# Performance work log

Measured on AMD Instinct MI355X. Metric: run time of the kernel, lower is better.

The kernel has to match this reference:

```python
import jax, jax.numpy as jnp
import numpy as np

E = 1024
FF = 4096
B, S = 4, 2048
EPS = 1e-5

def _layernorm(x, g, b):
    m = jnp.mean(x, axis=-1, keepdims=True)
    v = jnp.var(x, axis=-1, keepdims=True)
    return (x - m) * jax.lax.rsqrt(v + EPS) * g + b

def setup_inputs() -> dict:
    key = jax.random.key(0)
    ks = jax.random.split(key, 16)
    def lin(k, fan_in, shape):
        bound = 1.0 / np.sqrt(fan_in)
        return jax.random.uniform(k, shape, jnp.float32, -bound, bound)
    return {
        "src_embs": jax.random.normal(ks[0], (B, S, E), jnp.float32),
        "Wq_w": lin(ks[1], E, (E, E)), "Wq_b": lin(ks[2], E, (E,)),
        "Wk_w": lin(ks[3], E, (E, E)), "Wk_b": lin(ks[4], E, (E,)),
        "Wv_w": lin(ks[5], E, (E, E)), "Wv_b": lin(ks[6], E, (E,)),
        "Wo_w": lin(ks[7], E, (E, E)), "Wo_b": lin(ks[8], E, (E,)),
        "W1_w": lin(ks[9], E, (FF, E)), "W1_b": lin(ks[10], E, (FF,)),
        "W2_w": lin(ks[11], FF, (E, FF)), "W2_b": lin(ks[12], FF, (E,)),
        "g1": jnp.ones((E,), jnp.float32), "b1": jnp.zeros((E,), jnp.float32),
        "g2": jnp.ones((E,), jnp.float32), "b2": jnp.zeros((E,), jnp.float32),
        "g3": jnp.ones((E,), jnp.float32), "b3": jnp.zeros((E,), jnp.float32),
    }

def reference(src_embs, Wq_w, Wq_b, Wk_w, Wk_b, Wv_w, Wv_b, Wo_w, Wo_b,
              W1_w, W1_b, W2_w, W2_b, g1, b1, g2, b2, g3, b3):
    x = _layernorm(src_embs, g1, b1)
    Q = x @ Wq_w.T + Wq_b
    K = x @ Wk_w.T + Wk_b
    V = x @ Wv_w.T + Wv_b
    # single-head attention, scaled by sqrt(embed_dim) per source
    scores = jnp.einsum('bqe,bke->bqk', Q, K) / jnp.sqrt(jnp.float32(E))
    attn = jax.nn.softmax(scores, axis=-1)
    attn_out = jnp.einsum('bqk,bke->bqe', attn, V) @ Wo_w.T + Wo_b
    h = src_embs + attn_out
    hn = _layernorm(h, g2, b2)
    ff = jax.nn.relu(hn @ W1_w.T + W1_b) @ W2_w.T + W2_b
    out = h + ff
    return _layernorm(out, g3, b3)
```

## Files before the change

kernel.cpp:

```cpp
#include <hip/hip_runtime.h>
#include <cstdint>
#include <cmath>

#define E_DIM 1024
#define FF_DIM 4096
#define B_DIM 4
#define S_DIM 2048
#define NTOK (B_DIM * S_DIM)

typedef __bf16 bf16;
typedef __attribute__((ext_vector_type(8))) __bf16 bf16x8;
typedef __attribute__((ext_vector_type(4))) float f32x4;

__device__ __forceinline__ void gload_lds16(const void* g, void* l) {
  __builtin_amdgcn_global_load_lds(
      (const __attribute__((address_space(1))) unsigned int*)g,
      (__attribute__((address_space(3))) unsigned int*)l, 16, 0, 0);
}

__device__ __forceinline__ float waveRedSum(float v) {
#pragma unroll
  for (int o = 32; o > 0; o >>= 1) v += __shfl_xor(v, o, 64);
  return v;
}
__device__ __forceinline__ float waveRedMax(float v) {
#pragma unroll
  for (int o = 32; o > 0; o >>= 1) v = fmaxf(v, __shfl_xor(v, o, 64));
  return v;
}

__global__ __launch_bounds__(256) void cvt_k(const float* __restrict__ in,
                                             bf16* __restrict__ out, int n4) {
  int i = blockIdx.x * 256 + threadIdx.x;
  if (i < n4) {
    float4 v = reinterpret_cast<const float4*>(in)[i];
    bf16* o = out + (size_t)i * 4;
    o[0] = (bf16)v.x; o[1] = (bf16)v.y; o[2] = (bf16)v.z; o[3] = (bf16)v.w;
  }
}

template <typename OutT>
__global__ __launch_bounds__(256) void layernorm_k(const float* __restrict__ x,
                                                   OutT* __restrict__ out,
                                                   const float* __restrict__ g,
                                                   const float* __restrict__ b) {
  const int row = blockIdx.x;
  const int tid = threadIdx.x;
  const float4 v = reinterpret_cast<const float4*>(x + (size_t)row * E_DIM)[tid];
  float s = v.x + v.y + v.z + v.w;
  float q = v.x * v.x + v.y * v.y + v.z * v.z + v.w * v.w;
  s = waveRedSum(s);
  q = waveRedSum(q);
  __shared__ float sa[4], sb[4];
  const int lane = tid & 63, wid = tid >> 6;
  if (lane == 0) { sa[wid] = s; sb[wid] = q; }
  __syncthreads();
  s = sa[0] + sa[1] + sa[2] + sa[3];
  q = sb[0] + sb[1] + sb[2] + sb[3];
  const float mean = s * (1.0f / E_DIM);
  const float var = q * (1.0f / E_DIM) - mean * mean;
  const float rstd = rsqrtf(var + 1e-5f);
  const int c = tid * 4;
  OutT* op = out + (size_t)row * E_DIM + c;
  const float vv[4] = {v.x, v.y, v.z, v.w};
#pragma unroll
  for (int j = 0; j < 4; ++j)
    op[j] = (OutT)((vv[j] - mean) * rstd * g[c + j] + b[c + j]);
}

__global__ __launch_bounds__(256) void softmax_k(bf16* __restrict__ scores) {
  const int row = blockIdx.x;
  bf16* rp = scores + (size_t)row * S_DIM;
  const int tid = threadIdx.x;
  const int lane = tid & 63, wid = tid >> 6;
  bf16x8 v8 = *reinterpret_cast<const bf16x8*>(rp + tid * 8);
  float v[8];
#pragma unroll
  for (int j = 0; j < 8; ++j) v[j] = (float)v8[j];
  float mx = v[0];
#pragma unroll
  for (int j = 1; j < 8; ++j) mx = fmaxf(mx, v[j]);
  mx = waveRedMax(mx);
  __shared__ float sm_[4], ss_[4];
  if (lane == 0) sm_[wid] = mx;
  __syncthreads();
  mx = fmaxf(fmaxf(sm_[0], sm_[1]), fmaxf(sm_[2], sm_[3]));
  float e[8];
  float s = 0.f;
#pragma unroll
  for (int j = 0; j < 8; ++j) { e[j] = __expf(v[j] - mx); s += e[j]; }
  s = waveRedSum(s);
  if (lane == 0) ss_[wid] = s;
  __syncthreads();
  s = ss_[0] + ss_[1] + ss_[2] + ss_[3];
  const float inv = 1.0f / s;
  bf16x8 o;
#pragma unroll
  for (int j = 0; j < 8; ++j) o[j] = (bf16)(e[j] * inv);
  *reinterpret_cast<bf16x8*>(rp + tid * 8) = o;
}

__global__ __launch_bounds__(256) void transpose_k(const bf16* __restrict__ in,
                                                   bf16* __restrict__ out) {
  __shared__ bf16 t[32][33];
  const int b = blockIdx.z;
  const bf16* ip = in + (size_t)b * S_DIM * E_DIM;
  bf16* op = out + (size_t)b * S_DIM * E_DIM;
  const int e0 = blockIdx.x * 32, s0 = blockIdx.y * 32;
  const int tx = threadIdx.x & 31, ty = threadIdx.x >> 5;
#pragma unroll
  for (int r = 0; r < 32; r += 8) t[ty + r][tx] = ip[(size_t)(s0 + ty + r) * E_DIM + e0 + tx];
  __syncthreads();
#pragma unroll
  for (int r = 0; r < 32; r += 8) op[(size_t)(e0 + ty + r) * S_DIM + s0 + tx] = t[tx][ty + r];
}

__device__ __forceinline__ void stage_chunk(const bf16* __restrict__ A, int lda,
                                            const bf16* __restrict__ Bt, int ldb,
                                            char* smem, int m0, int n0, int t,
                                            int c, int tid, int wid) {
  const int rb = t % 3;
  const int kk = t * 64;
  const int r = tid >> 3;
  const int col8 = (tid & 7) ^ (r & 7);
  if (c < 4) {
    gload_lds16(A + (size_t)(m0 + c * 64 + r) * lda + kk + col8 * 8,
                smem + rb * 32768 + c * 8192 + wid * 1024);
  } else {
    gload_lds16(Bt + (size_t)(n0 + (c - 4) * 64 + r) * ldb + kk + col8 * 8,
                smem + 98304 + rb * 16384 + (c - 4) * 8192 + wid * 1024);
  }
}

template <typename OutT, bool RELU>
__global__ __launch_bounds__(512) void gemm256_k(
    const bf16* __restrict__ A0, int lda, const bf16* __restrict__ Bt0, int ldb,
    OutT* __restrict__ C0, int ldc, int M, int N, int K,
    const float* __restrict__ bias, const float* __restrict__ resid, int ldr,
    float scale, size_t sAz, size_t sBz, size_t sCz) {
  __shared__ __align__(16) char smem[147456];
  const int tid = threadIdx.x;
  const int lane = tid & 63;
  const int wid = tid >> 6;
  const int wr = wid >> 2;
  const int wc = wid & 3;

  const bf16* A = A0 + (size_t)blockIdx.z * sAz;
  const bf16* Bt = Bt0 + (size_t)blockIdx.z * sBz;
  OutT* C = C0 + (size_t)blockIdx.z * sCz;

  const int gx = gridDim.x;
  const int nwg = gx * gridDim.y;
  int wg = blockIdx.y * gx + blockIdx.x;
  {
    const int q = nwg >> 3, r8 = nwg & 7;
    const int xcd = wg & 7, lin = wg >> 3;
    wg = (xcd < r8 ? xcd * (q + 1) : r8 * (q + 1) + (xcd - r8) * q) + lin;
  }
  const int m0 = (wg / gx) * 256;
  const int n0 = (wg % gx) * 128;

  f32x4 acc[2][4][2] = {};

#pragma unroll
  for (int c = 0; c < 6; ++c) stage_chunk(A, lda, Bt, ldb, smem, m0, n0, 0, c, tid, wid);
#pragma unroll
  for (int c = 0; c < 6; ++c) stage_chunk(A, lda, Bt, ldb, smem, m0, n0, 1, c, tid, wid);
  asm volatile("s_waitcnt vmcnt(6)" ::: "memory");
  __builtin_amdgcn_s_barrier();

  const int NT = K >> 6;
  for (int t = 0; t < NT; ++t) {
    const int rb = t % 3;
    const char* lA = smem + rb * 32768;
    const char* lB = smem + 98304 + rb * 16384;
#pragma unroll
    for (int mh = 0; mh < 2; ++mh) {
      bf16x8 af[4][2], bfv[2][2];
#pragma unroll
      for (int fm = 0; fm < 4; ++fm) {
        const int row = wr * 128 + mh * 64 + fm * 16 + (lane & 15);
#pragma unroll
        for (int ks = 0; ks < 2; ++ks) {
          const int g = ((ks << 2) | (lane >> 4)) ^ (row & 7);
          af[fm][ks] = *reinterpret_cast<const bf16x8*>(lA + row * 128 + g * 16);
        }
      }
#pragma unroll
      for (int fn = 0; fn < 2; ++fn) {
        const int row = wc * 32 + fn * 16 + (lane & 15);
#pragma unroll
        for (int ks = 0; ks < 2; ++ks) {
          const int g = ((ks << 2) | (lane >> 4)) ^ (row & 7);
          bfv[fn][ks] = *reinterpret_cast<const bf16x8*>(lB + row * 128 + g * 16);
        }
      }
      if (t + 2 < NT) {
#pragma unroll
        for (int c = 0; c < 3; ++c)
          stage_chunk(A, lda, Bt, ldb, smem, m0, n0, t + 2, mh * 3 + c, tid, wid);
      }
      __builtin_amdgcn_s_barrier();
      __builtin_amdgcn_s_setprio(1);
#pragma unroll
      for (int fm = 0; fm < 4; ++fm)
#pragma unroll
        for (int fn = 0; fn < 2; ++fn) {
          acc[mh][fm][fn] = __builtin_amdgcn_mfma_f32_16x16x32_bf16(
              af[fm][0], bfv[fn][0], acc[mh][fm][fn], 0, 0, 0);
          acc[mh][fm][fn] = __builtin_amdgcn_mfma_f32_16x16x32_bf16(
              af[fm][1], bfv[fn][1], acc[mh][fm][fn], 0, 0, 0);
        }
      __builtin_amdgcn_s_setprio(0);
      if (mh == 1) {
        if (t + 2 < NT) {
          asm volatile("s_waitcnt vmcnt(6)" ::: "memory");
        } else {
          asm volatile("s_waitcnt vmcnt(0)" ::: "memory");
        }
      }
      __builtin_amdgcn_s_barrier();
    }
  }

#pragma unroll
  for (int mh = 0; mh < 2; ++mh)
#pragma unroll
    for (int fn = 0; fn < 2; ++fn) {
      const int col = n0 + wc * 32 + fn * 16 + (lane & 15);
      const float bv = bias ? bias[col] : 0.0f;
#pragma unroll
      for (int fm = 0; fm < 4; ++fm)
#pragma unroll
        for (int i = 0; i < 4; ++i) {
          const int row = m0 + wr * 128 + mh * 64 + fm * 16 + (lane >> 4) * 4 + i;
          float v = acc[mh][fm][fn][i] * scale + bv;
          if (resid) v += resid[(size_t)row * ldr + col];
          if (RELU) v = fmaxf(v, 0.0f);
          C[(size_t)row * ldc + col] = (OutT)v;
        }
    }
}

extern "C" void kernel_launch(void* const* d_in, const int* in_sizes, int n_in,
                              void* d_out, int out_size, void* d_ws,
                              size_t ws_size, hipStream_t stream) {
  const float* src = (const float*)d_in[0];
  const float* Wq_w = (const float*)d_in[1];
  const float* Wq_b = (const float*)d_in[2];
  const float* Wk_w = (const float*)d_in[3];
  const float* Wk_b = (const float*)d_in[4];
  const float* Wv_w = (const float*)d_in[5];
  const float* Wv_b = (const float*)d_in[6];
  const float* Wo_w = (const float*)d_in[7];
  const float* Wo_b = (const float*)d_in[8];
  const float* W1_w = (const float*)d_in[9];
  const float* W1_b = (const float*)d_in[10];
  const float* W2_w = (const float*)d_in[11];
  const float* W2_b = (const float*)d_in[12];
  const float* g1 = (const float*)d_in[13];
  const float* b1 = (const float*)d_in[14];
  const float* g2 = (const float*)d_in[15];
  const float* b2 = (const float*)d_in[16];
  const float* g3 = (const float*)d_in[17];
  const float* b3 = (const float*)d_in[18];
  float* out = (float*)d_out;
  (void)ws_size; (void)in_sizes; (void)n_in; (void)out_size;

  const size_t MB = 1ull << 20;
  char* ws = (char*)d_ws;
  bf16* wq = (bf16*)(ws + 0 * MB);
  bf16* wk = (bf16*)(ws + 2 * MB);
  bf16* wv = (bf16*)(ws + 4 * MB);
  bf16* wo = (bf16*)(ws + 6 * MB);
  bf16* w1 = (bf16*)(ws + 8 * MB);
  bf16* w2 = (bf16*)(ws + 16 * MB);
  bf16* Qb = (bf16*)(ws + 24 * MB);
  bf16* Kb = (bf16*)(ws + 40 * MB);
  bf16* Vb = (bf16*)(ws + 56 * MB);
  bf16* Vt = (bf16*)(ws + 72 * MB);
  bf16* scoresB = (bf16*)(ws + 88 * MB);
  bf16* xln = (bf16*)(ws + 88 * MB);
  bf16* ctx = Qb;
  bf16* hn = Kb;
  bf16* f1 = Vb;
  float* h = out;

  cvt_k<<<(E_DIM * E_DIM / 4 + 255) / 256, 256, 0, stream>>>(Wq_w, wq, E_DIM * E_DIM / 4);
  cvt_k<<<(E_DIM * E_DIM / 4 + 255) / 256, 256, 0, stream>>>(Wk_w, wk, E_DIM * E_DIM / 4);
  cvt_k<<<(E_DIM * E_DIM / 4 + 255) / 256, 256, 0, stream>>>(Wv_w, wv, E_DIM * E_DIM / 4);
  cvt_k<<<(E_DIM * E_DIM / 4 + 255) / 256, 256, 0, stream>>>(Wo_w, wo, E_DIM * E_DIM / 4);
  cvt_k<<<(FF_DIM * E_DIM / 4 + 255) / 256, 256, 0, stream>>>(W1_w, w1, FF_DIM * E_DIM / 4);
  cvt_k<<<(FF_DIM * E_DIM / 4 + 255) / 256, 256, 0, stream>>>(W2_w, w2, FF_DIM * E_DIM / 4);

  layernorm_k<bf16><<<NTOK, 256, 0, stream>>>(src, xln, g1, b1);

  dim3 gQKV(E_DIM / 128, NTOK / 256);
  gemm256_k<bf16, false><<<gQKV, 512, 0, stream>>>(xln, E_DIM, wq, E_DIM, Qb, E_DIM,
      NTOK, E_DIM, E_DIM, Wq_b, nullptr, 0, 1.0f, 0, 0, 0);
  gemm256_k<bf16, false><<<gQKV, 512, 0, stream>>>(xln, E_DIM, wk, E_DIM, Kb, E_DIM,
      NTOK, E_DIM, E_DIM, Wk_b, nullptr, 0, 1.0f, 0, 0, 0);
  gemm256_k<bf16, false><<<gQKV, 512, 0, stream>>>(xln, E_DIM, wv, E_DIM, Vb, E_DIM,
      NTOK, E_DIM, E_DIM, Wv_b, nullptr, 0, 1.0f, 0, 0, 0);

  dim3 gSc(S_DIM / 128, S_DIM / 256, B_DIM);
  gemm256_k<bf16, false><<<gSc, 512, 0, stream>>>(
      Qb, E_DIM, Kb, E_DIM, scoresB, S_DIM, S_DIM, S_DIM, E_DIM,
      nullptr, nullptr, 0, 1.0f / 32.0f,
      (size_t)S_DIM * E_DIM, (size_t)S_DIM * E_DIM, (size_t)S_DIM * S_DIM);

  softmax_k<<<B_DIM * S_DIM, 256, 0, stream>>>(scoresB);

  transpose_k<<<dim3(E_DIM / 32, S_DIM / 32, B_DIM), 256, 0, stream>>>(Vb, Vt);

  dim3 gPV(E_DIM / 128, S_DIM / 256, B_DIM);
  gemm256_k<bf16, false><<<gPV, 512, 0, stream>>>(
      scoresB, S_DIM, Vt, S_DIM, ctx, E_DIM, S_DIM, E_DIM, S_DIM,
      nullptr, nullptr, 0, 1.0f,
      (size_t)S_DIM * S_DIM, (size_t)S_DIM * E_DIM, (size_t)S_DIM * E_DIM);

  gemm256_k<float, false><<<gQKV, 512, 0, stream>>>(ctx, E_DIM, wo, E_DIM, h, E_DIM,
      NTOK, E_DIM, E_DIM, Wo_b, src, E_DIM, 1.0f, 0, 0, 0);

  layernorm_k<bf16><<<NTOK, 256, 0, stream>>>(h, hn, g2, b2);

  dim3 gF1(FF_DIM / 128, NTOK / 256);
  gemm256_k<bf16, true><<<gF1, 512, 0, stream>>>(hn, E_DIM, w1, E_DIM, f1, FF_DIM,
      NTOK, FF_DIM, E_DIM, W1_b, nullptr, 0, 1.0f, 0, 0, 0);

  gemm256_k<float, false><<<gQKV, 512, 0, stream>>>(f1, FF_DIM, w2, FF_DIM, out, E_DIM,
      NTOK, E_DIM, FF_DIM, W2_b, h, E_DIM, 1.0f, 0, 0, 0);

  layernorm_k<float><<<NTOK, 256, 0, stream>>>(out, out, g3, b3);
}
```

Before: 453.1 us.

## Fuse QKV projections into one GEMM and add 256-wide N tiles

Concatenates the Q, K and V weights and biases so a single GEMM produces a packed QKV buffer, and reads the score GEMM and V transpose directly from it through strides. The GEMM kernel is templated on N tile width (128 or 256), with the K step cut to 32 and a new LDS swizzle. The 256-wide tile is used for QKV, scores and FFN1. Larger tiles improve operand reuse and cut launches, but they use more registers and produce fewer workgroups, and the buffer aliasing changes (hn, f1, ctx) must not overlap live data.

```diff
diff --git a/kernel.cpp b/kernel.cpp
--- a/kernel.cpp
+++ b/kernel.cpp
@@ -7,6 +7,7 @@
 #define B_DIM 4
 #define S_DIM 2048
 #define NTOK (B_DIM * S_DIM)
+#define QKV_N 3072
 
 typedef __bf16 bf16;
 typedef __attribute__((ext_vector_type(8))) __bf16 bf16x8;
@@ -101,49 +102,44 @@
 }
 
 __global__ __launch_bounds__(256) void transpose_k(const bf16* __restrict__ in,
+                                                   int ld_in, size_t bstride_in,
                                                    bf16* __restrict__ out) {
   __shared__ bf16 t[32][33];
   const int b = blockIdx.z;
-  const bf16* ip = in + (size_t)b * S_DIM * E_DIM;
+  const bf16* ip = in + (size_t)b * bstride_in;
   bf16* op = out + (size_t)b * S_DIM * E_DIM;
   const int e0 = blockIdx.x * 32, s0 = blockIdx.y * 32;
   const int tx = threadIdx.x & 31, ty = threadIdx.x >> 5;
 #pragma unroll
-  for (int r = 0; r < 32; r += 8) t[ty + r][tx] = ip[(size_t)(s0 + ty + r) * E_DIM + e0 + tx];
+  for (int r = 0; r < 32; r += 8)
+    t[ty + r][tx] = ip[(size_t)(s0 + ty + r) * ld_in + e0 + tx];
   __syncthreads();
 #pragma unroll
-  for (int r = 0; r < 32; r += 8) op[(size_t)(e0 + ty + r) * S_DIM + s0 + tx] = t[tx][ty + r];
-}
-
-__device__ __forceinline__ void stage_chunk(const bf16* __restrict__ A, int lda,
-                                            const bf16* __restrict__ Bt, int ldb,
-                                            char* smem, int m0, int n0, int t,
-                                            int c, int tid, int wid) {
-  const int rb = t % 3;
-  const int kk = t * 64;
-  const int r = tid >> 3;
-  const int col8 = (tid & 7) ^ (r & 7);
-  if (c < 4) {
-    gload_lds16(A + (size_t)(m0 + c * 64 + r) * lda + kk + col8 * 8,
-                smem + rb * 32768 + c * 8192 + wid * 1024);
-  } else {
-    gload_lds16(Bt + (size_t)(n0 + (c - 4) * 64 + r) * ldb + kk + col8 * 8,
-                smem + 98304 + rb * 16384 + (c - 4) * 8192 + wid * 1024);
-  }
-}
-
-template <typename OutT, bool RELU>
+  for (int r = 0; r < 32; r += 8)
+    op[(size_t)(e0 + ty + r) * S_DIM + s0 + tx] = t[tx][ty + r];
+}
+
+template <int BN, typename OutT, bool RELU>
 __global__ __launch_bounds__(512) void gemm256_k(
     const bf16* __restrict__ A0, int lda, const bf16* __restrict__ Bt0, int ldb,
     OutT* __restrict__ C0, int ldc, int M, int N, int K,
     const float* __restrict__ bias, const float* __restrict__ resid, int ldr,
     float scale, size_t sAz, size_t sBz, size_t sCz) {
-  __shared__ __align__(16) char smem[147456];
+  constexpr int WC = BN / 64;
+  constexpr int WR = 8 / WC;
+  constexpr int MSPAN = 256 / WR;
+  constexpr int FM = MSPAN / 16;
+  constexpr int NPH = (BN == 256) ? 2 : 1;
+  constexpr int CPT = 2 + BN / 128;
+  constexpr int ACH = 1024;
+  constexpr int TILE_B = (256 + BN) * 64;
+  __shared__ __align__(16) char smem[3 * TILE_B];
+
   const int tid = threadIdx.x;
   const int lane = tid & 63;
   const int wid = tid >> 6;
-  const int wr = wid >> 2;
-  const int wc = wid & 3;
+  const int wr = wid / WC;
+  const int wc = wid % WC;
 
   const bf16* A = A0 + (size_t)blockIdx.z * sAz;
   const bf16* Bt = Bt0 + (size_t)blockIdx.z * sBz;
@@ -158,63 +154,79 @@
     wg = (xcd < r8 ? xcd * (q + 1) : r8 * (q + 1) + (xcd - r8) * q) + lin;
   }
   const int m0 = (wg / gx) * 256;
-  const int n0 = (wg % gx) * 128;
-
-  f32x4 acc[2][4][2] = {};
-
-#pragma unroll
-  for (int c = 0; c < 6; ++c) stage_chunk(A, lda, Bt, ldb, smem, m0, n0, 0, c, tid, wid);
-#pragma unroll
-  for (int c = 0; c < 6; ++c) stage_chunk(A, lda, Bt, ldb, smem, m0, n0, 1, c, tid, wid);
-  asm volatile("s_waitcnt vmcnt(6)" ::: "memory");
+  const int n0 = (wg % gx) * BN;
+
+  auto stage_chunk = [&](int t, int c) {
+    const int rb = t % 3;
+    const int ci = c * 512 + tid;
+    char* base = smem + rb * TILE_B;
+    if (ci < ACH) {
+      const int row = ci >> 2, g = (ci & 3) ^ ((row >> 1) & 3);
+      gload_lds16(A + (size_t)(m0 + row) * lda + t * 32 + g * 8,
+                  base + (c * 512 + wid * 64) * 16);
+    } else {
+      const int cb = ci - ACH;
+      const int row = cb >> 2, g = (cb & 3) ^ ((row >> 1) & 3);
+      gload_lds16(Bt + (size_t)(n0 + row) * ldb + t * 32 + g * 8,
+                  base + (c * 512 + wid * 64) * 16);
+    }
+  };
+
+  f32x4 acc[FM][4] = {};
+
+  const int NT = K >> 5;
+#pragma unroll
+  for (int c = 0; c < CPT; ++c) stage_chunk(0, c);
+#pragma unroll
+  for (int c = 0; c < CPT; ++c) stage_chunk(1, c);
+  if constexpr (CPT == 4) asm volatile("s_waitcnt vmcnt(4)" ::: "memory");
+  else                    asm volatile("s_waitcnt vmcnt(3)" ::: "memory");
   __builtin_amdgcn_s_barrier();
 
-  const int NT = K >> 6;
   for (int t = 0; t < NT; ++t) {
     const int rb = t % 3;
-    const char* lA = smem + rb * 32768;
-    const char* lB = smem + 98304 + rb * 16384;
-#pragma unroll
-    for (int mh = 0; mh < 2; ++mh) {
-      bf16x8 af[4][2], bfv[2][2];
-#pragma unroll
-      for (int fm = 0; fm < 4; ++fm) {
-        const int row = wr * 128 + mh * 64 + fm * 16 + (lane & 15);
-#pragma unroll
-        for (int ks = 0; ks < 2; ++ks) {
-          const int g = ((ks << 2) | (lane >> 4)) ^ (row & 7);
-          af[fm][ks] = *reinterpret_cast<const bf16x8*>(lA + row * 128 + g * 16);
+    const char* lA = smem + rb * TILE_B;
+    const char* lB = lA + 256 * 64;
+    bf16x8 bfv[4];
+    bf16x8 af[4];
+#pragma unroll
+    for (int p = 0; p < NPH; ++p) {
+      if (p == 0) {
+#pragma unroll
+        for (int fn = 0; fn < 4; ++fn) {
+          const int row = wc * 64 + fn * 16 + (lane & 15);
+          const int g = (lane >> 4) ^ ((row >> 1) & 3);
+          bfv[fn] = *reinterpret_cast<const bf16x8*>(lB + row * 64 + g * 16);
         }
       }
 #pragma unroll
-      for (int fn = 0; fn < 2; ++fn) {
-        const int row = wc * 32 + fn * 16 + (lane & 15);
-#pragma unroll
-        for (int ks = 0; ks < 2; ++ks) {
-          const int g = ((ks << 2) | (lane >> 4)) ^ (row & 7);
-          bfv[fn][ks] = *reinterpret_cast<const bf16x8*>(lB + row * 128 + g * 16);
+      for (int f4 = 0; f4 < 4; ++f4) {
+        const int row = wr * MSPAN + (p * 4 + f4) * 16 + (lane & 15);
+        const int g = (lane >> 4) ^ ((row >> 1) & 3);
+        af[f4] = *reinterpret_cast<const bf16x8*>(lA + row * 64 + g * 16);
+      }
+      if (t + 2 < NT) {
+        if constexpr (NPH == 2) {
+          stage_chunk(t + 2, p * 2);
+          stage_chunk(t + 2, p * 2 + 1);
+        } else {
+#pragma unroll
+          for (int c = 0; c < CPT; ++c) stage_chunk(t + 2, c);
         }
-      }
-      if (t + 2 < NT) {
-#pragma unroll
-        for (int c = 0; c < 3; ++c)
-          stage_chunk(A, lda, Bt, ldb, smem, m0, n0, t + 2, mh * 3 + c, tid, wid);
       }
       __builtin_amdgcn_s_barrier();
       __builtin_amdgcn_s_setprio(1);
 #pragma unroll
-      for (int fm = 0; fm < 4; ++fm)
-#pragma unroll
-        for (int fn = 0; fn < 2; ++fn) {
-          acc[mh][fm][fn] = __builtin_amdgcn_mfma_f32_16x16x32_bf16(
-              af[fm][0], bfv[fn][0], acc[mh][fm][fn], 0, 0, 0);
-          acc[mh][fm][fn] = __builtin_amdgcn_mfma_f32_16x16x32_bf16(
-              af[fm][1], bfv[fn][1], acc[mh][fm][fn], 0, 0, 0);
-        }
+      for (int f4 = 0; f4 < 4; ++f4)
+#pragma unroll
+        for (int fn = 0; fn < 4; ++fn)
+          acc[p * 4 + f4][fn] = __builtin_amdgcn_mfma_f32_16x16x32_bf16(
+              af[f4], bfv[fn], acc[p * 4 + f4][fn], 0, 0, 0);
       __builtin_amdgcn_s_setprio(0);
-      if (mh == 1) {
+      if (p == NPH - 1) {
         if (t + 2 < NT) {
-          asm volatile("s_waitcnt vmcnt(6)" ::: "memory");
+          if constexpr (CPT == 4) asm volatile("s_waitcnt vmcnt(4)" ::: "memory");
+          else                    asm volatile("s_waitcnt vmcnt(3)" ::: "memory");
         } else {
           asm volatile("s_waitcnt vmcnt(0)" ::: "memory");
         }
@@ -224,22 +236,20 @@
   }
 
 #pragma unroll
-  for (int mh = 0; mh < 2; ++mh)
-#pragma unroll
-    for (int fn = 0; fn < 2; ++fn) {
-      const int col = n0 + wc * 32 + fn * 16 + (lane & 15);
-      const float bv = bias ? bias[col] : 0.0f;
-#pragma unroll
-      for (int fm = 0; fm < 4; ++fm)
-#pragma unroll
-        for (int i = 0; i < 4; ++i) {
-          const int row = m0 + wr * 128 + mh * 64 + fm * 16 + (lane >> 4) * 4 + i;
-          float v = acc[mh][fm][fn][i] * scale + bv;
-          if (resid) v += resid[(size_t)row * ldr + col];
-          if (RELU) v = fmaxf(v, 0.0f);
-          C[(size_t)row * ldc + col] = (OutT)v;
-        }
-    }
+  for (int fn = 0; fn < 4; ++fn) {
+    const int col = n0 + wc * 64 + fn * 16 + (lane & 15);
+    const float bv = bias ? bias[col] : 0.0f;
+#pragma unroll
+    for (int fm = 0; fm < FM; ++fm)
+#pragma unroll
+      for (int i = 0; i < 4; ++i) {
+        const int row = m0 + wr * MSPAN + fm * 16 + (lane >> 4) * 4 + i;
+        float v = acc[fm][fn][i] * scale + bv;
+        if (resid) v += resid[(size_t)row * ldr + col];
+        if (RELU) v = fmaxf(v, 0.0f);
+        C[(size_t)row * ldc + col] = (OutT)v;
+      }
+  }
 }
 
 extern "C" void kernel_launch(void* const* d_in, const int* in_sizes, int n_in,
@@ -269,67 +279,70 @@
 
   const size_t MB = 1ull << 20;
   char* ws = (char*)d_ws;
-  bf16* wq = (bf16*)(ws + 0 * MB);
-  bf16* wk = (bf16*)(ws + 2 * MB);
-  bf16* wv = (bf16*)(ws + 4 * MB);
+  bf16* wqkv = (bf16*)(ws + 0 * MB);
   bf16* wo = (bf16*)(ws + 6 * MB);
   bf16* w1 = (bf16*)(ws + 8 * MB);
   bf16* w2 = (bf16*)(ws + 16 * MB);
-  bf16* Qb = (bf16*)(ws + 24 * MB);
-  bf16* Kb = (bf16*)(ws + 40 * MB);
-  bf16* Vb = (bf16*)(ws + 56 * MB);
+  bf16* Cqkv = (bf16*)(ws + 24 * MB);
   bf16* Vt = (bf16*)(ws + 72 * MB);
   bf16* scoresB = (bf16*)(ws + 88 * MB);
   bf16* xln = (bf16*)(ws + 88 * MB);
-  bf16* ctx = Qb;
-  bf16* hn = Kb;
-  bf16* f1 = Vb;
+  float* bqkv = (float*)(ws + 104 * MB);
+  bf16* ctx = Cqkv;
+  bf16* hn = scoresB;
+  bf16* f1 = (bf16*)(ws + 24 * MB);
   float* h = out;
 
-  cvt_k<<<(E_DIM * E_DIM / 4 + 255) / 256, 256, 0, stream>>>(Wq_w, wq, E_DIM * E_DIM / 4);
-  cvt_k<<<(E_DIM * E_DIM / 4 + 255) / 256, 256, 0, stream>>>(Wk_w, wk, E_DIM * E_DIM / 4);
-  cvt_k<<<(E_DIM * E_DIM / 4 + 255) / 256, 256, 0, stream>>>(Wv_w, wv, E_DIM * E_DIM / 4);
+  cvt_k<<<(E_DIM * E_DIM / 4 + 255) / 256, 256, 0, stream>>>(Wq_w, wqkv, E_DIM * E_DIM / 4);
+  cvt_k<<<(E_DIM * E_DIM / 4 + 255) / 256, 256, 0, stream>>>(Wk_w, wqkv + (size_t)E_DIM * E_DIM, E_DIM * E_DIM / 4);
+  cvt_k<<<(E_DIM * E_DIM / 4 + 255) / 256, 256, 0, stream>>>(Wv_w, wqkv + 2 * (size_t)E_DIM * E_DIM, E_DIM * E_DIM / 4);
   cvt_k<<<(E_DIM * E_DIM / 4 + 255) / 256, 256, 0, stream>>>(Wo_w, wo, E_DIM * E_DIM / 4);
   cvt_k<<<(FF_DIM * E_DIM / 4 + 255) / 256, 256, 0, stream>>>(W1_w, w1, FF_DIM * E_DIM / 4);
   cvt_k<<<(FF_DIM * E_DIM / 4 + 255) / 256, 256, 0, stream>>>(W2_w, w2, FF_DIM * E_DIM / 4);
+  hipMemcpyAsync(bqkv, Wq_b, E_DIM * 4, hipMemcpyDeviceToDevice, stream);
+  hipMemcpyAsync(bqkv + E_DIM, Wk_b, E_DIM * 4, hipMemcpyDeviceToDevice, stream);
+  hipMemcpyAsync(bqkv + 2 * E_DIM, Wv_b, E_DIM * 4, hipMemcpyDeviceToDevice, stream);
 
   layernorm_k<bf16><<<NTOK, 256, 0, stream>>>(src, xln, g1, b1);
 
-  dim3 gQKV(E_DIM / 128, NTOK / 256);
-  gemm256_k<bf16, false><<<gQKV, 512, 0, stream>>>(xln, E_DIM, wq, E_DIM, Qb, E_DIM,
-      NTOK, E_DIM, E_DIM, Wq_b, nullptr, 0, 1.0f, 0, 0, 0);
-  gemm256_k<bf16, false><<<gQKV, 512, 0, stream>>>(xln, E_DIM, wk, E_DIM, Kb, E_DIM,
-      NTOK, E_DIM, E_DIM, Wk_b, nullptr, 0, 1.0f, 0, 0, 0);
-  gemm256_k<bf16, false><<<gQKV, 512, 0, stream>>>(xln, E_DIM, wv, E_DIM, Vb, E_DIM,
-      NTOK, E_DIM, E_DIM, Wv_b, nullptr, 0, 1.0f, 0, 0, 0);
-
-  dim3 gSc(S_DIM / 128, S_DIM / 256, B_DIM);
-  gemm256_k<bf16, false><<<gSc, 512, 0, stream>>>(
-      Qb, E_DIM, Kb, E_DIM, scoresB, S_DIM, S_DIM, S_DIM, E_DIM,
+  dim3 gQKV(QKV_N / 256, NTOK / 256);
+  gemm256_k<256, bf16, false><<<gQKV, 512, 0, stream>>>(
+      xln, E_DIM, wqkv, E_DIM, Cqkv, QKV_N, NTOK, QKV_N, E_DIM,
+      bqkv, nullptr, 0, 1.0f, 0, 0, 0);
+
+  dim3 gSc(S_DIM / 256, S_DIM / 256, B_DIM);
+  gemm256_k<256, bf16, false><<<gSc, 512, 0, stream>>>(
+      Cqkv, QKV_N, Cqkv + E_DIM, QKV_N, scoresB, S_DIM, S_DIM, S_DIM, E_DIM,
       nullptr, nullptr, 0, 1.0f / 32.0f,
-      (size_t)S_DIM * E_DIM, (size_t)S_DIM * E_DIM, (size_t)S_DIM * S_DIM);
+      (size_t)S_DIM * QKV_N, (size_t)S_DIM * QKV_N, (size_t)S_DIM * S_DIM);
 
   softmax_k<<<B_DIM * S_DIM, 256, 0, stream>>>(scoresB);
 
-  transpose_k<<<dim3(E_DIM / 32, S_DIM / 32, B_DIM), 256, 0, stream>>>(Vb, Vt);
+  transpose_k<<<dim3(E_DIM / 32, S_DIM / 32, B_DIM), 256, 0, stream>>>(
+      Cqkv + 2 * E_DIM, QKV_N, (size_t)S_DIM * QKV_N, Vt);
 
   dim3 gPV(E_DIM / 128, S_DIM / 256, B_DIM);
-  gemm256_k<bf16, false><<<gPV, 512, 0, stream>>>(
+  gemm256_k<128, bf16, false><<<gPV, 512, 0, stream>>>(
       scoresB, S_DIM, Vt, S_DIM, ctx, E_DIM, S_DIM, E_DIM, S_DIM,
       nullptr, nullptr, 0, 1.0f,
       (size_t)S_DIM * S_DIM, (size_t)S_DIM * E_DIM, (size_t)S_DIM * E_DIM);
 
-  gemm256_k<float, false><<<gQKV, 512, 0, stream>>>(ctx, E_DIM, wo, E_DIM, h, E_DIM,
-      NTOK, E_DIM, E_DIM, Wo_b, src, E_DIM, 1.0f, 0, 0, 0);
+  dim3 gWo(E_DIM / 128, NTOK / 256);
+  gemm256_k<128, float, false><<<gWo, 512, 0, stream>>>(
+      ctx, E_DIM, wo, E_DIM, h, E_DIM, NTOK, E_DIM, E_DIM,
+      Wo_b, src, E_DIM, 1.0f, 0, 0, 0);
 
   layernorm_k<bf16><<<NTOK, 256, 0, stream>>>(h, hn, g2, b2);
 
-  dim3 gF1(FF_DIM / 128, NTOK / 256);
-  gemm256_k<bf16, true><<<gF1, 512, 0, stream>>>(hn, E_DIM, w1, E_DIM, f1, FF_DIM,
-      NTOK, FF_DIM, E_DIM, W1_b, nullptr, 0, 1.0f, 0, 0, 0);
-
-  gemm256_k<float, false><<<gQKV, 512, 0, stream>>>(f1, FF_DIM, w2, FF_DIM, out, E_DIM,
-      NTOK, E_DIM, FF_DIM, W2_b, h, E_DIM, 1.0f, 0, 0, 0);
+  dim3 gF1(FF_DIM / 256, NTOK / 256);
+  gemm256_k<256, bf16, true><<<gF1, 512, 0, stream>>>(
+      hn, E_DIM, w1, E_DIM, f1, FF_DIM, NTOK, FF_DIM, E_DIM,
+      W1_b, nullptr, 0, 1.0f, 0, 0, 0);
+
+  dim3 gF2(E_DIM / 128, NTOK / 256);
+  gemm256_k<128, float, false><<<gF2, 512, 0, stream>>>(
+      f1, FF_DIM, w2, FF_DIM, out, E_DIM, NTOK, E_DIM, FF_DIM,
+      W2_b, h, E_DIM, 1.0f, 0, 0, 0);
 
   layernorm_k<float><<<NTOK, 256, 0, stream>>>(out, out, g3, b3);
 }
```

Measured after the change: 456.7 us. Within noise of the previous version (+0.8%).
